# Kernel tuning notes

Measured on AMD Instinct MI355X. Metric: run time of the kernel, lower is better.

## Reference

```python
import jax, jax.numpy as jnp
import numpy as np

B, T, E, H = 256, 256, 384, 64

def setup_inputs() -> dict:
    key = jax.random.key(0)
    ks = jax.random.split(key, 4)
    s = 1.0 / np.sqrt(E)
    return {
        "x":  jax.random.normal(ks[0], (B, T, E), dtype=jnp.float32),
        "Wq": jax.random.normal(ks[1], (E, H), dtype=jnp.float32) * s,
        "bq": jnp.zeros((H,), dtype=jnp.float32),
        "Wk": jax.random.normal(ks[2], (E, H), dtype=jnp.float32) * s,
        "bk": jnp.zeros((H,), dtype=jnp.float32),
        "Wv": jax.random.normal(ks[3], (E, H), dtype=jnp.float32) * s,
        "bv": jnp.zeros((H,), dtype=jnp.float32),
    }

def reference(x, Wq, bq, Wk, bk, Wv, bv):
    # QKV projections: [B,T,E] @ [E,H] -> [B,T,H]
    q = x @ Wq + bq
    k = x @ Wk + bk
    v = x @ Wv + bv
    # attention scores (NOTE: original has no 1/sqrt(d) scaling)
    wei = jnp.einsum('bth,bsh->bts', q, k)  # [B,T,T]
    causal = jnp.tril(jnp.ones((T, T), dtype=bool))
    wei = jnp.where(causal, wei, -jnp.inf)
    wei = jax.nn.softmax(wei, axis=-1)
    # dropout is identity in eval mode
    out = jnp.einsum('bts,bsh->bth', wei, v)  # [B,T,H]
    return out
```

## Files before the change

### kernel.cpp

```cpp
#include <hip/hip_runtime.h>
#include <math.h>

#define Bb 256
#define Tt 256
#define Ee 384
#define Hh 64

typedef __attribute__((ext_vector_type(8))) short bf16x8;
typedef __attribute__((ext_vector_type(4))) float f32x4;
typedef __attribute__((ext_vector_type(4))) unsigned int u32x4;

__device__ inline short f2bf(float f) {
    unsigned u = __float_as_uint(f);
    u += 0x7FFFu + ((u >> 16) & 1);
    return (short)(u >> 16);
}
__device__ inline float bf2f(short s) {
    return __uint_as_float(((unsigned)(unsigned short)s) << 16);
}
__device__ inline unsigned cvt_pk_bf16(float a, float b) {
    unsigned r;
    asm("v_cvt_pk_bf16_f32 %0, %1, %2" : "=v"(r) : "v"(a), "v"(b));
    return r;
}

#define MFMA16(a, b, c) __builtin_amdgcn_mfma_f32_16x16x32_bf16((a), (b), (c), 0, 0, 0)

#define WLO_OFF 147456

#define BB0 65536
#define K_HI 0
#define K_LO 32768
#define VF   65536
#define QH   98304
#define QL   116736
#define PBASE 98304
#define SMEM_BYTES 135168

__global__ __launch_bounds__(256) void prep_w(
    const float* __restrict__ Wq, const float* __restrict__ Wk,
    const float* __restrict__ Wv, unsigned char* __restrict__ wsp)
{
    __shared__ float wlds[32 * 66];
    const int bid = blockIdx.x;
    const int ec  = bid / 3, m = bid - ec * 3;
    const float* Wm = (m == 0) ? Wq : (m == 1 ? Wk : Wv);
    const int tid = threadIdx.x;

    const float4* src = reinterpret_cast<const float4*>(Wm + ec * 2048) + tid * 2;
    float4 a = src[0], b = src[1];
    int f = tid * 8;
    float* d = wlds + (f >> 6) * 66 + (f & 63);
    d[0] = a.x; d[1] = a.y; d[2] = a.z; d[3] = a.w;
    d[4] = b.x; d[5] = b.y; d[6] = b.z; d[7] = b.w;
    __syncthreads();

    const int tl = tid >> 6, lu = tid & 63;
    const int koct = lu >> 4, n = lu & 15;
    const int c = tl * 16 + n;
    bf16x8 hi8, lo8;
    #pragma unroll
    for (int j = 0; j < 8; ++j) {
        float v = wlds[(koct * 8 + j) * 66 + c];
        short h = f2bf(v);
        hi8[j] = h;
        lo8[j] = f2bf(v - bf2f(h));
    }
    const int frag = ec * 12 + m * 4 + tl;
    *reinterpret_cast<bf16x8*>(wsp + frag * 1024 + lu * 16) = hi8;
    *reinterpret_cast<bf16x8*>(wsp + WLO_OFF + frag * 1024 + lu * 16) = lo8;
}

__global__ __launch_bounds__(1024) void head_fused(
    const float* __restrict__ x,
    const float* __restrict__ bq, const float* __restrict__ bk,
    const float* __restrict__ bv,
    const unsigned char* __restrict__ wsp,
    float* __restrict__ out)
{
    __shared__ __align__(16) unsigned char smem[SMEM_BYTES];

    const int b    = blockIdx.x;
    const int tid  = threadIdx.x;
    const int w    = tid >> 6;
    const int lane = tid & 63;
    const int quad = lane >> 4;
    const int nl   = lane & 15;
    const int ri   = w >> 2;
    const int cj   = w & 3;

    f32x4 acc[4][3];
    #pragma unroll
    for (int i = 0; i < 4; ++i)
        #pragma unroll
        for (int j = 0; j < 3; ++j) acc[i][j] = (f32x4){0,0,0,0};

    const float4* x4 = reinterpret_cast<const float4*>(x + (size_t)b * Tt * Ee);

    auto bgld = [&](int ecn) {
        if (w < 12) {
            int p = ecn & 1;
            const unsigned char* ghi = wsp + (size_t)(ecn * 12 + w) * 1024 + (size_t)lane * 16;
            const unsigned char* glo = ghi + WLO_OFF;
            __builtin_amdgcn_global_load_lds(
                (const __attribute__((address_space(1))) unsigned*)ghi,
                (__attribute__((address_space(3))) unsigned*)(smem + BB0 + p * 24576 + w * 1024),
                16, 0, 0);
            __builtin_amdgcn_global_load_lds(
                (const __attribute__((address_space(1))) unsigned*)glo,
                (__attribute__((address_space(3))) unsigned*)(smem + BB0 + p * 24576 + 12288 + w * 1024),
                16, 0, 0);
        }
    };

    const int pt = tid & 255;
    const float4* xp = x4 + pt * 96;
    unsigned char* adst = smem + (pt >> 4) * 1024 + (pt & 15) * 16;
    float4 px[8];

    auto loadX = [&](int ecsrc) {
        const float4* xr_ = xp + ecsrc * 8;
        #pragma unroll
        for (int j = 0; j < 8; ++j) px[j] = xr_[j];
    };
    auto stageWrite = [&](int nb) {
        #pragma unroll
        for (int ko = 0; ko < 4; ++ko) {
            float v0 = px[2*ko+0].x, v1 = px[2*ko+0].y,
                  v2 = px[2*ko+0].z, v3 = px[2*ko+0].w,
                  v4 = px[2*ko+1].x, v5 = px[2*ko+1].y,
                  v6 = px[2*ko+1].z, v7 = px[2*ko+1].w;
            unsigned h0 = cvt_pk_bf16(v0, v1);
            unsigned h1 = cvt_pk_bf16(v2, v3);
            unsigned h2 = cvt_pk_bf16(v4, v5);
            unsigned h3 = cvt_pk_bf16(v6, v7);
            unsigned l0 = cvt_pk_bf16(v0 - __uint_as_float(h0 << 16),
                                      v1 - __uint_as_float(h0 & 0xFFFF0000u));
            unsigned l1 = cvt_pk_bf16(v2 - __uint_as_float(h1 << 16),
                                      v3 - __uint_as_float(h1 & 0xFFFF0000u));
            unsigned l2 = cvt_pk_bf16(v4 - __uint_as_float(h2 << 16),
                                      v5 - __uint_as_float(h2 & 0xFFFF0000u));
            unsigned l3 = cvt_pk_bf16(v6 - __uint_as_float(h3 << 16),
                                      v7 - __uint_as_float(h3 & 0xFFFF0000u));
            u32x4 hv = {h0, h1, h2, h3};
            u32x4 lv = {l0, l1, l2, l3};
            *reinterpret_cast<u32x4*>(adst + nb + ko * 256) = hv;
            *reinterpret_cast<u32x4*>(adst + nb + 16384 + ko * 256) = lv;
        }
    };

    bgld(0);
    if (w >= 12) {
        loadX(0);
        stageWrite(0);
        loadX(1);
    }

    for (int ec = 0; ec < 12; ++ec) {
        __syncthreads();
        if (w < 12) {
            if (ec < 11) bgld(ec + 1);
        } else {
            if (ec < 11) stageWrite((1 - (ec & 1)) * 32768);
            if (ec < 10) loadX(ec + 2);
        }

        const int ab = (ec & 1) * 32768;
        const int bb = BB0 + (ec & 1) * 24576;
        bf16x8 bh[3], bl[3];
        #pragma unroll
        for (int ct = 0; ct < 3; ++ct) {
            int o = bb + (cj * 3 + ct) * 1024 + lane * 16;
            bh[ct] = *reinterpret_cast<bf16x8*>(smem + o);
            bl[ct] = *reinterpret_cast<bf16x8*>(smem + o + 12288);
        }
        __builtin_amdgcn_s_setprio(1);
        #pragma unroll
        for (int rt = 0; rt < 4; ++rt) {
            int ao = ab + (4 * ri + rt) * 1024 + lane * 16;
            bf16x8 ah = *reinterpret_cast<bf16x8*>(smem + ao);
            bf16x8 al = *reinterpret_cast<bf16x8*>(smem + ao + 16384);
            #pragma unroll
            for (int ct = 0; ct < 3; ++ct) {
                acc[rt][ct] = MFMA16(ah, bh[ct], acc[rt][ct]);
                acc[rt][ct] = MFMA16(al, bh[ct], acc[rt][ct]);
                acc[rt][ct] = MFMA16(ah, bl[ct], acc[rt][ct]);
            }
        }
        __builtin_amdgcn_s_setprio(0);
    }
    __syncthreads();

    #pragma unroll
    for (int ct = 0; ct < 3; ++ct) {
        int col = (cj * 3 + ct) * 16 + nl;
        float bias = (col < 64) ? bq[col] : (col < 128 ? bk[col - 64] : bv[col - 128]);
        #pragma unroll
        for (int rt = 0; rt < 4; ++rt)
            #pragma unroll
            for (int r = 0; r < 4; ++r) acc[rt][ct][r] += bias;
    }

    #pragma unroll
    for (int ct = 0; ct < 3; ++ct) {
        int col = (cj * 3 + ct) * 16 + nl;
        #pragma unroll
        for (int rt = 0; rt < 4; ++rt) {
            #pragma unroll
            for (int r = 0; r < 4; ++r) {
                float val = acc[rt][ct][r];
                int s = ri * 64 + rt * 16 + quad * 4 + r;
                if (col >= 64 && col < 128) {
                    int h = col - 64;
                    int addr = ((s >> 4) * 2 + (h >> 5)) * 1024
                             + ((((h & 31) >> 3) * 16 + (s & 15)) * 8 + (h & 7)) * 2;
                    short hi = f2bf(val);
                    short lo = f2bf(val - bf2f(hi));
                    *reinterpret_cast<short*>(smem + K_HI + addr) = hi;
                    *reinterpret_cast<short*>(smem + K_LO + addr) = lo;
                } else if (col >= 128) {
                    int h = col - 128, sl = s & 31;
                    int addr = ((s >> 5) * 4 + (h >> 4)) * 1024
                             + (((sl >> 3) * 16 + (h & 15)) * 8 + (sl & 7)) * 2;
                    *reinterpret_cast<short*>(smem + VF + addr) = f2bf(val);
                }
            }
        }
    }

    auto writeQhalf = [&]() {
        #pragma unroll
        for (int ct = 0; ct < 3; ++ct) {
            int col = (cj * 3 + ct) * 16 + nl;
            if (col < 64) {
                #pragma unroll
                for (int rt = 0; rt < 4; ++rt) {
                    #pragma unroll
                    for (int r = 0; r < 4; ++r) {
                        float val = acc[rt][ct][r];
                        int s = ri * 64 + rt * 16 + quad * 4 + r;
                        int rloc = s & 127;
                        short hi = f2bf(val);
                        short lo = f2bf(val - bf2f(hi));
                        *reinterpret_cast<short*>(smem + QH + (rloc * 72 + col) * 2) = hi;
                        *reinterpret_cast<short*>(smem + QL + (rloc * 72 + col) * 2) = lo;
                    }
                }
            }
        }
    };
    bf16x8 qh0, qh1, ql0, ql1;
    auto readQ = [&]() {
        int rloc = (16 * w + nl) & 127;
        int base = rloc * 144;
        qh0 = *reinterpret_cast<bf16x8*>(smem + QH + base + quad * 16);
        qh1 = *reinterpret_cast<bf16x8*>(smem + QH + base + 64 + quad * 16);
        ql0 = *reinterpret_cast<bf16x8*>(smem + QL + base + quad * 16);
        ql1 = *reinterpret_cast<bf16x8*>(smem + QL + base + 64 + quad * 16);
    };

    if (ri < 2) writeQhalf();
    __syncthreads();
    if (w < 8) readQ();
    __syncthreads();
    if (ri >= 2) writeQhalf();
    __syncthreads();
    if (w >= 8) readQ();
    __syncthreads();

    f32x4 oacc[4];
    #pragma unroll
    for (int i = 0; i < 4; ++i) oacc[i] = (f32x4){0,0,0,0};
    float lsum4[4] = {0.f, 0.f, 0.f, 0.f};
    const int t0 = w * 16;
    unsigned char* pb = smem + PBASE + w * 1344;
    const int npairs = (w >> 1) + 1;

    bf16x8 kA0, kA1, kA2, kA3, kB0, kB1, kB2, kB3;
#define LDK(P) do {                                                     \
        int kb0_ = (2 * (P)) * 2048 + lane * 16;                        \
        kA0 = *reinterpret_cast<bf16x8*>(smem + K_HI + kb0_);           \
        kA1 = *reinterpret_cast<bf16x8*>(smem + K_HI + kb0_ + 1024);    \
        kA2 = *reinterpret_cast<bf16x8*>(smem + K_LO + kb0_);           \
        kA3 = *reinterpret_cast<bf16x8*>(smem + K_LO + kb0_ + 1024);    \
        kB0 = *reinterpret_cast<bf16x8*>(smem + K_HI + kb0_ + 2048);    \
        kB1 = *reinterpret_cast<bf16x8*>(smem + K_HI + kb0_ + 3072);    \
        kB2 = *reinterpret_cast<bf16x8*>(smem + K_LO + kb0_ + 2048);    \
        kB3 = *reinterpret_cast<bf16x8*>(smem + K_LO + kb0_ + 3072);    \
    } while (0)

    LDK(0);
    for (int p = 0; p < npairs; ++p) {
        f32x4 sa0 = (f32x4){0,0,0,0}, sa1 = (f32x4){0,0,0,0};
        f32x4 sb0 = (f32x4){0,0,0,0}, sb1 = (f32x4){0,0,0,0};
        __builtin_amdgcn_s_setprio(1);
        sa0 = MFMA16(qh0, kA0, sa0);  sb0 = MFMA16(qh0, kB0, sb0);
        sa1 = MFMA16(qh1, kA1, sa1);  sb1 = MFMA16(qh1, kB1, sb1);
        sa0 = MFMA16(ql0, kA0, sa0);  sb0 = MFMA16(ql0, kB0, sb0);
        sa1 = MFMA16(ql1, kA1, sa1);  sb1 = MFMA16(ql1, kB1, sb1);
        sa0 = MFMA16(qh0, kA2, sa0);  sb0 = MFMA16(qh0, kB2, sb0);
        sa1 = MFMA16(qh1, kA3, sa1);  sb1 = MFMA16(qh1, kB3, sb1);
        __builtin_amdgcn_s_setprio(0);

        float rs[4];
        const int sg0 = 32 * p + nl, sg1 = sg0 + 16;
        #pragma unroll
        for (int r = 0; r < 4; ++r) {
            int tg = t0 + quad * 4 + r;
            float sva = sa0[r] + sa1[r];
            float svb = sb0[r] + sb1[r];
            float pva = (sg0 <= tg) ? __expf(sva) : 0.f;
            float pvb = (sg1 <= tg) ? __expf(svb) : 0.f;
            rs[r] = pva + pvb;
            *reinterpret_cast<short*>(pb + ((quad * 4 + r) * 40 + nl) * 2)      = f2bf(pva);
            *reinterpret_cast<short*>(pb + ((quad * 4 + r) * 40 + 16 + nl) * 2) = f2bf(pvb);
        }
        asm volatile("" ::: "memory");
        bf16x8 pa  = *reinterpret_cast<bf16x8*>(pb + (nl * 40 + quad * 8) * 2);
        int vb = p * 4096 + lane * 16;
        bf16x8 vf0 = *reinterpret_cast<bf16x8*>(smem + VF + vb);
        bf16x8 vf1 = *reinterpret_cast<bf16x8*>(smem + VF + vb + 1024);
        bf16x8 vf2 = *reinterpret_cast<bf16x8*>(smem + VF + vb + 2048);
        bf16x8 vf3 = *reinterpret_cast<bf16x8*>(smem + VF + vb + 3072);
        if (p + 1 < npairs) LDK(p + 1);

        #pragma unroll
        for (int r = 0; r < 4; ++r) {
            float v = rs[r];
            v += __shfl_xor(v, 1);
            v += __shfl_xor(v, 2);
            v += __shfl_xor(v, 4);
            v += __shfl_xor(v, 8);
            lsum4[r] += v;
        }
        __builtin_amdgcn_s_setprio(1);
        oacc[0] = MFMA16(pa, vf0, oacc[0]);
        oacc[1] = MFMA16(pa, vf1, oacc[1]);
        oacc[2] = MFMA16(pa, vf2, oacc[2]);
        oacc[3] = MFMA16(pa, vf3, oacc[3]);
        __builtin_amdgcn_s_setprio(0);
    }
#undef LDK

    float* ob = out + (size_t)b * Tt * Hh + (size_t)t0 * Hh;
    #pragma unroll
    for (int r = 0; r < 4; ++r) {
        float inv = 1.0f / lsum4[r];
        #pragma unroll
        for (int nt = 0; nt < 4; ++nt)
            ob[(quad * 4 + r) * 64 + nt * 16 + nl] = oacc[nt][r] * inv;
    }
}

extern "C" void kernel_launch(void* const* d_in, const int* in_sizes, int n_in,
                              void* d_out, int out_size, void* d_ws, size_t ws_size,
                              hipStream_t stream) {
    const float* x  = (const float*)d_in[0];
    const float* Wq = (const float*)d_in[1];
    const float* bq = (const float*)d_in[2];
    const float* Wk = (const float*)d_in[3];
    const float* bk = (const float*)d_in[4];
    const float* Wv = (const float*)d_in[5];
    const float* bv = (const float*)d_in[6];
    float* out = (float*)d_out;
    unsigned char* wsp = (unsigned char*)d_ws;
    hipLaunchKernelGGL(prep_w, dim3(36), dim3(256), 0, stream, Wq, Wk, Wv, wsp);
    hipLaunchKernelGGL(head_fused, dim3(Bb), dim3(1024), 0, stream,
                       x, bq, bk, bv, wsp, out);
}
```

Baseline: 188.3 us.

## Split fused head kernel into QKV projection and attention kernels via workspace

Replaces the single per-batch fused kernel (256 blocks of 1024 threads with a large LDS footprint) with two kernels. Each kernel uses 512 blocks of 512 threads, splitting every batch across two blocks. The first computes the QKV projection in split-bf16 MFMA with a double-buffered pipeline and writes pre-swizzled Q/K/V fragments to workspace. The second does causal attention per 16-row tile, reading K/V directly from global/L2 with small LDS. The aim is more parallelism and occupancy than the one-block-per-batch design, at the cost of a round trip of about 40 MB through HBM/L2 and an extra launch; it falls back to the fused kernel if the workspace is too small.

```diff
diff --git a/kernel.cpp b/kernel.cpp
--- a/kernel.cpp
+++ b/kernel.cpp
@@ -27,6 +27,10 @@
 #define MFMA16(a, b, c) __builtin_amdgcn_mfma_f32_16x16x32_bf16((a), (b), (c), 0, 0, 0)
 
 #define WLO_OFF 147456
+
+#define WQKV 294912
+#define SB   163840
+#define WS_NEED (294912ull + 256ull * 163840ull)
 
 #define BB0 65536
 #define K_HI 0
@@ -69,6 +73,292 @@
     const int frag = ec * 12 + m * 4 + tl;
     *reinterpret_cast<bf16x8*>(wsp + frag * 1024 + lu * 16) = hi8;
     *reinterpret_cast<bf16x8*>(wsp + WLO_OFF + frag * 1024 + lu * 16) = lo8;
+}
+
+#define BBA 32768
+__global__ __launch_bounds__(512, 4) void qkv_proj(
+    const float* __restrict__ x,
+    const float* __restrict__ bq, const float* __restrict__ bk,
+    const float* __restrict__ bv,
+    const unsigned char* __restrict__ wsp,
+    unsigned char* __restrict__ qkvws)
+{
+    __shared__ __align__(16) unsigned char smem[81920];
+
+    const int bid  = blockIdx.x;
+    const int b    = bid >> 1;
+    const int half = bid & 1;
+    const int tid  = threadIdx.x;
+    const int w    = tid >> 6;
+    const int lane = tid & 63;
+    const int quad = lane >> 4;
+    const int nl   = lane & 15;
+    const int ri   = w >> 1;
+    const int cj   = w & 1;
+
+    f32x4 acc[2][6];
+    #pragma unroll
+    for (int i = 0; i < 2; ++i)
+        #pragma unroll
+        for (int j = 0; j < 6; ++j) acc[i][j] = (f32x4){0,0,0,0};
+
+    const float4* x4 = reinterpret_cast<const float4*>(x + (size_t)b * Tt * Ee);
+
+    auto bgld = [&](int ecn) {
+        if (w < 6) {
+            int p = ecn & 1;
+            int f0 = w * 2;
+            const unsigned char* g0 = wsp + (size_t)(ecn * 12 + f0) * 1024 + (size_t)lane * 16;
+            unsigned char* d0 = smem + BBA + p * 24576 + f0 * 1024;
+            __builtin_amdgcn_global_load_lds(
+                (const __attribute__((address_space(1))) unsigned*)g0,
+                (__attribute__((address_space(3))) unsigned*)d0, 16, 0, 0);
+            __builtin_amdgcn_global_load_lds(
+                (const __attribute__((address_space(1))) unsigned*)(g0 + 1024),
+                (__attribute__((address_space(3))) unsigned*)(d0 + 1024), 16, 0, 0);
+            __builtin_amdgcn_global_load_lds(
+                (const __attribute__((address_space(1))) unsigned*)(g0 + WLO_OFF),
+                (__attribute__((address_space(3))) unsigned*)(d0 + 12288), 16, 0, 0);
+            __builtin_amdgcn_global_load_lds(
+                (const __attribute__((address_space(1))) unsigned*)(g0 + WLO_OFF + 1024),
+                (__attribute__((address_space(3))) unsigned*)(d0 + 12288 + 1024), 16, 0, 0);
+        }
+    };
+
+    const int pt = tid & 127;
+    const float4* xp = x4 + (half * 128 + pt) * 96;
+    unsigned char* adst = smem + (pt >> 4) * 1024 + (pt & 15) * 16;
+
+    auto stageA = [&](int ecsrc, int nb) {
+        float4 px[8];
+        const float4* xr_ = xp + ecsrc * 8;
+        #pragma unroll
+        for (int j = 0; j < 8; ++j) px[j] = xr_[j];
+        #pragma unroll
+        for (int ko = 0; ko < 4; ++ko) {
+            float v0 = px[2*ko+0].x, v1 = px[2*ko+0].y,
+                  v2 = px[2*ko+0].z, v3 = px[2*ko+0].w,
+                  v4 = px[2*ko+1].x, v5 = px[2*ko+1].y,
+                  v6 = px[2*ko+1].z, v7 = px[2*ko+1].w;
+            unsigned h0 = cvt_pk_bf16(v0, v1);
+            unsigned h1 = cvt_pk_bf16(v2, v3);
+            unsigned h2 = cvt_pk_bf16(v4, v5);
+            unsigned h3 = cvt_pk_bf16(v6, v7);
+            unsigned l0 = cvt_pk_bf16(v0 - __uint_as_float(h0 << 16),
+                                      v1 - __uint_as_float(h0 & 0xFFFF0000u));
+            unsigned l1 = cvt_pk_bf16(v2 - __uint_as_float(h1 << 16),
+                                      v3 - __uint_as_float(h1 & 0xFFFF0000u));
+            unsigned l2 = cvt_pk_bf16(v4 - __uint_as_float(h2 << 16),
+                                      v5 - __uint_as_float(h2 & 0xFFFF0000u));
+            unsigned l3 = cvt_pk_bf16(v6 - __uint_as_float(h3 << 16),
+                                      v7 - __uint_as_float(h3 & 0xFFFF0000u));
+            u32x4 hv = {h0, h1, h2, h3};
+            u32x4 lv = {l0, l1, l2, l3};
+            *reinterpret_cast<u32x4*>(adst + nb + ko * 256) = hv;
+            *reinterpret_cast<u32x4*>(adst + nb + 8192 + ko * 256) = lv;
+        }
+    };
+
+    bgld(0);
+    if (w >= 6) stageA(0, 0);
+
+    for (int ec = 0; ec < 12; ++ec) {
+        __syncthreads();
+        if (w < 6) {
+            if (ec < 11) bgld(ec + 1);
+        } else {
+            if (ec < 11) stageA(ec + 1, (1 - (ec & 1)) * 16384);
+        }
+
+        const int ab = (ec & 1) * 16384;
+        const int bb = BBA + (ec & 1) * 24576;
+        bf16x8 bh[6], bl[6];
+        #pragma unroll
+        for (int ct = 0; ct < 6; ++ct) {
+            int o = bb + (cj * 6 + ct) * 1024 + lane * 16;
+            bh[ct] = *reinterpret_cast<bf16x8*>(smem + o);
+            bl[ct] = *reinterpret_cast<bf16x8*>(smem + o + 12288);
+        }
+        __builtin_amdgcn_s_setprio(1);
+        #pragma unroll
+        for (int rt = 0; rt < 2; ++rt) {
+            int ao = ab + (ri * 2 + rt) * 1024 + lane * 16;
+            bf16x8 ah = *reinterpret_cast<bf16x8*>(smem + ao);
+            bf16x8 al = *reinterpret_cast<bf16x8*>(smem + ao + 8192);
+            #pragma unroll
+            for (int ct = 0; ct < 6; ++ct) {
+                acc[rt][ct] = MFMA16(ah, bh[ct], acc[rt][ct]);
+                acc[rt][ct] = MFMA16(al, bh[ct], acc[rt][ct]);
+                acc[rt][ct] = MFMA16(ah, bl[ct], acc[rt][ct]);
+            }
+        }
+        __builtin_amdgcn_s_setprio(0);
+    }
+    __syncthreads();
+
+    #pragma unroll
+    for (int ct = 0; ct < 6; ++ct) {
+        int col = (cj * 6 + ct) * 16 + nl;
+        float bias = (col < 64) ? bq[col] : (col < 128 ? bk[col - 64] : bv[col - 128]);
+        #pragma unroll
+        for (int rt = 0; rt < 2; ++rt)
+            #pragma unroll
+            for (int r = 0; r < 4; ++r) acc[rt][ct][r] += bias;
+    }
+
+    #pragma unroll
+    for (int ct = 0; ct < 6; ++ct) {
+        int col = (cj * 6 + ct) * 16 + nl;
+        #pragma unroll
+        for (int rt = 0; rt < 2; ++rt) {
+            #pragma unroll
+            for (int r = 0; r < 4; ++r) {
+                float val = acc[rt][ct][r];
+                int sl = ri * 32 + rt * 16 + quad * 4 + r;
+                if (col < 64) {
+                    short hi = f2bf(val);
+                    short lo = f2bf(val - bf2f(hi));
+                    int qaddr = (sl * 64 + col) * 2;
+                    *reinterpret_cast<short*>(smem + 49152 + qaddr) = hi;
+                    *reinterpret_cast<short*>(smem + 65536 + qaddr) = lo;
+                } else if (col < 128) {
+                    int h = col - 64;
+                    int addr = ((sl >> 4) * 2 + (h >> 5)) * 1024
+                             + ((((h & 31) >> 3) * 16 + (sl & 15)) * 8 + (h & 7)) * 2;
+                    short hi = f2bf(val);
+                    short lo = f2bf(val - bf2f(hi));
+                    *reinterpret_cast<short*>(smem + addr) = hi;
+                    *reinterpret_cast<short*>(smem + 16384 + addr) = lo;
+                } else {
+                    int h = col - 128, sll = sl & 31;
+                    int addr = ((sl >> 5) * 4 + (h >> 4)) * 1024
+                             + (((sll >> 3) * 16 + (h & 15)) * 8 + (sll & 7)) * 2;
+                    *reinterpret_cast<short*>(smem + 32768 + addr) = f2bf(val);
+                }
+            }
+        }
+    }
+    __syncthreads();
+
+    unsigned char* dstb = qkvws + (size_t)b * SB;
+    #pragma unroll
+    for (int it = 0; it < 10; ++it) {
+        int L = it * 8192 + tid * 16;
+        u32x4 v = *reinterpret_cast<u32x4*>(smem + L);
+        *reinterpret_cast<u32x4*>(dstb + (L >> 14) * 32768 + half * 16384 + (L & 16383)) = v;
+    }
+}
+
+__global__ __launch_bounds__(512, 4) void attn(
+    const unsigned char* __restrict__ qkvws, float* __restrict__ out)
+{
+    __shared__ __align__(16) unsigned char smem[10752];
+
+    const int bid  = blockIdx.x;
+    const int b    = bid >> 1;
+    const int half = bid & 1;
+    const int tid  = threadIdx.x;
+    const int w    = tid >> 6;
+    const int lane = tid & 63;
+    const int quad = lane >> 4;
+    const int nl   = lane & 15;
+    const int g    = half * 8 + w;
+    const int t0   = g * 16;
+
+    const unsigned char* kvq = qkvws + (size_t)b * SB;
+    const unsigned char* KHg = kvq;
+    const unsigned char* KLg = kvq + 32768;
+    const unsigned char* VVg = kvq + 65536;
+    const unsigned char* QHg = kvq + 98304;
+    const unsigned char* QLg = kvq + 131072;
+
+    const int qb = (t0 + nl) * 128 + quad * 16;
+    bf16x8 qh0 = *reinterpret_cast<const bf16x8*>(QHg + qb);
+    bf16x8 qh1 = *reinterpret_cast<const bf16x8*>(QHg + qb + 64);
+    bf16x8 ql0 = *reinterpret_cast<const bf16x8*>(QLg + qb);
+    bf16x8 ql1 = *reinterpret_cast<const bf16x8*>(QLg + qb + 64);
+
+    f32x4 oacc[4];
+    #pragma unroll
+    for (int i = 0; i < 4; ++i) oacc[i] = (f32x4){0,0,0,0};
+    float lsum4[4] = {0.f, 0.f, 0.f, 0.f};
+    unsigned char* pb = smem + w * 1344;
+    const int npairs = (g >> 1) + 1;
+
+    bf16x8 kA0, kA1, kA2, kA3, kB0, kB1, kB2, kB3;
+#define LDK(P) do {                                                       \
+        int kb_ = (2 * (P)) * 2048 + lane * 16;                           \
+        kA0 = *reinterpret_cast<const bf16x8*>(KHg + kb_);                \
+        kA1 = *reinterpret_cast<const bf16x8*>(KHg + kb_ + 1024);         \
+        kA2 = *reinterpret_cast<const bf16x8*>(KLg + kb_);                \
+        kA3 = *reinterpret_cast<const bf16x8*>(KLg + kb_ + 1024);         \
+        kB0 = *reinterpret_cast<const bf16x8*>(KHg + kb_ + 2048);         \
+        kB1 = *reinterpret_cast<const bf16x8*>(KHg + kb_ + 3072);         \
+        kB2 = *reinterpret_cast<const bf16x8*>(KLg + kb_ + 2048);         \
+        kB3 = *reinterpret_cast<const bf16x8*>(KLg + kb_ + 3072);         \
+    } while (0)
+
+    LDK(0);
+    for (int p = 0; p < npairs; ++p) {
+        f32x4 sa0 = (f32x4){0,0,0,0}, sa1 = (f32x4){0,0,0,0};
+        f32x4 sb0 = (f32x4){0,0,0,0}, sb1 = (f32x4){0,0,0,0};
+        __builtin_amdgcn_s_setprio(1);
+        sa0 = MFMA16(qh0, kA0, sa0);  sb0 = MFMA16(qh0, kB0, sb0);
+        sa1 = MFMA16(qh1, kA1, sa1);  sb1 = MFMA16(qh1, kB1, sb1);
+        sa0 = MFMA16(ql0, kA0, sa0);  sb0 = MFMA16(ql0, kB0, sb0);
+        sa1 = MFMA16(ql1, kA1, sa1);  sb1 = MFMA16(ql1, kB1, sb1);
+        sa0 = MFMA16(qh0, kA2, sa0);  sb0 = MFMA16(qh0, kB2, sb0);
+        sa1 = MFMA16(qh1, kA3, sa1);  sb1 = MFMA16(qh1, kB3, sb1);
+        __builtin_amdgcn_s_setprio(0);
+
+        float rs[4];
+        const int sg0 = 32 * p + nl, sg1 = sg0 + 16;
+        #pragma unroll
+        for (int r = 0; r < 4; ++r) {
+            int tg = t0 + quad * 4 + r;
+            float sva = sa0[r] + sa1[r];
+            float svb = sb0[r] + sb1[r];
+            float pva = (sg0 <= tg) ? __expf(sva) : 0.f;
+            float pvb = (sg1 <= tg) ? __expf(svb) : 0.f;
+            rs[r] = pva + pvb;
+            *reinterpret_cast<short*>(pb + ((quad * 4 + r) * 40 + nl) * 2)      = f2bf(pva);
+            *reinterpret_cast<short*>(pb + ((quad * 4 + r) * 40 + 16 + nl) * 2) = f2bf(pvb);
+        }
+        asm volatile("" ::: "memory");
+        bf16x8 pa  = *reinterpret_cast<bf16x8*>(pb + (nl * 40 + quad * 8) * 2);
+        int vb = p * 4096 + lane * 16;
+        bf16x8 vf0 = *reinterpret_cast<const bf16x8*>(VVg + vb);
+        bf16x8 vf1 = *reinterpret_cast<const bf16x8*>(VVg + vb + 1024);
+        bf16x8 vf2 = *reinterpret_cast<const bf16x8*>(VVg + vb + 2048);
+        bf16x8 vf3 = *reinterpret_cast<const bf16x8*>(VVg + vb + 3072);
+        if (p + 1 < npairs) LDK(p + 1);
+
+        #pragma unroll
+        for (int r = 0; r < 4; ++r) {
+            float v = rs[r];
+            v += __shfl_xor(v, 1);
+            v += __shfl_xor(v, 2);
+            v += __shfl_xor(v, 4);
+            v += __shfl_xor(v, 8);
+            lsum4[r] += v;
+        }
+        __builtin_amdgcn_s_setprio(1);
+        oacc[0] = MFMA16(pa, vf0, oacc[0]);
+        oacc[1] = MFMA16(pa, vf1, oacc[1]);
+        oacc[2] = MFMA16(pa, vf2, oacc[2]);
+        oacc[3] = MFMA16(pa, vf3, oacc[3]);
+        __builtin_amdgcn_s_setprio(0);
+    }
+#undef LDK
+
+    float* ob = out + (size_t)b * Tt * Hh + (size_t)t0 * Hh;
+    #pragma unroll
+    for (int r = 0; r < 4; ++r) {
+        float inv = 1.0f / lsum4[r];
+        #pragma unroll
+        for (int nt = 0; nt < 4; ++nt)
+            ob[(quad * 4 + r) * 64 + nt * 16 + nl] = oacc[nt][r] * inv;
+    }
 }
 
 __global__ __launch_bounds__(1024) void head_fused(
@@ -365,6 +655,13 @@
     float* out = (float*)d_out;
     unsigned char* wsp = (unsigned char*)d_ws;
     hipLaunchKernelGGL(prep_w, dim3(36), dim3(256), 0, stream, Wq, Wk, Wv, wsp);
-    hipLaunchKernelGGL(head_fused, dim3(Bb), dim3(1024), 0, stream,
-                       x, bq, bk, bv, wsp, out);
-}
+    if (ws_size >= WS_NEED) {
+        hipLaunchKernelGGL(qkv_proj, dim3(512), dim3(512), 0, stream,
+                           x, bq, bk, bv, wsp, wsp + WQKV);
+        hipLaunchKernelGGL(attn, dim3(512), dim3(512), 0, stream,
+                           wsp + WQKV, out);
+    } else {
+        hipLaunchKernelGGL(head_fused, dim3(Bb), dim3(1024), 0, stream,
+                           x, bq, bk, bv, wsp, out);
+    }
+}
```

Result: slower. 193.8 us (+2.9%).
